# Optimization experiments

Hardware: AMD Instinct MI355X
Metric: run time of the kernel (lower is better)

Reference implementation:

```python
import jax, jax.numpy as jnp
import numpy as np

DT = 10.0          # ms per step
T_STEPS = 120      # rollout length
THRESHOLD = 0.5
MIX = 0.0          # competition_mix (buffer, default 0.0)
EPS_TOTAL = 1e-6
EPS_SLOPE = 1e-3
NOISE_SEED = 42


def setup_inputs() -> dict:
    key = jax.random.key(0)
    B, C = 65536, 4
    logits = jax.random.normal(key, (B, C), dtype=jnp.float32)
    return {
        "logits": logits,
        "input_scale": jnp.float32(0.25),
        "leak": jnp.full((C,), 0.08, dtype=jnp.float32),
        "self_excitation": jnp.full((C,), 0.12, dtype=jnp.float32),
        "inhibition": jnp.float32(0.08),
        "competition_gain": jnp.float32(1.0),
        "noise_std": jnp.float32(0.02),
        "evidence_w": jnp.float32(1.0),   # evidence_proj: Linear(1,1) weight
        "evidence_b": jnp.float32(0.0),   # evidence_proj bias
    }


def _forward(logits, input_scale, leak, self_excitation, inhibition,
             competition_gain, noise_std, evidence_w, evidence_b):
    B, C = logits.shape
    # momentary evidence: scale, center, softplus, 1x1 linear
    centered = logits * input_scale
    centered = centered - jnp.mean(centered, axis=1, keepdims=True)
    evidence = jax.nn.softplus(centered) * evidence_w + evidence_b  # (B, C)

    lk = jax.nn.softplus(leak)                # (C,)
    se = jax.nn.softplus(self_excitation)     # (C,)
    inhib = jax.nn.softplus(inhibition)       # ()
    cgain = jax.nn.softplus(competition_gain) # ()
    nstd = jax.nn.softplus(noise_std)         # ()

    keys = jax.random.split(jax.random.key(NOISE_SEED), T_STEPS)

    def step(acc, k):
        total = jnp.sum(acc, axis=1, keepdims=True)      # (B, 1)
        total_other = total - acc                        # (B, C)
        normalized_other = total_other / (total + EPS_TOTAL)
        competition = (1.0 - MIX) * total_other + MIX * cgain * normalized_other
        drive = evidence + se * acc - inhib * competition - lk * acc
        noise = jax.random.normal(k, (B, C), dtype=jnp.float32) * nstd
        dsdt = jax.nn.softplus(drive + noise) - acc
        acc_new = jnp.maximum(acc + 0.2 * dsdt, 0.0)     # clamp(min=0)
        return acc_new, (acc_new, dsdt)

    acc0 = jnp.zeros((B, C), dtype=jnp.float32)
    _, (traj, dsdt_traj) = jax.lax.scan(step, acc0, keys)
    traj = jnp.transpose(traj, (1, 0, 2))           # (B, T, C)
    dsdt_traj = jnp.transpose(dsdt_traj, (1, 0, 2)) # (B, T, C)

    # DiffDecisionMultiClass: first threshold crossing per class, with
    # linear interpolation using dsdt (slope = 0.2*dsdt per step) so the
    # decision time is differentiable via the implicit-function gradient.
    diff = traj - THRESHOLD                          # (B, T, C)
    crossed = diff > 0.0
    any_c = jnp.any(crossed, axis=1)                 # (B, C)
    idx = jnp.argmax(crossed, axis=1)                # (B, C) first crossing step
    idx = jnp.where(any_c, idx, T_STEPS - 1)

    diff_c = jnp.take_along_axis(diff, idx[:, None, :], axis=1)[:, 0, :]       # (B, C)
    slope = 0.2 * jnp.take_along_axis(dsdt_traj, idx[:, None, :], axis=1)[:, 0, :]
    slope_safe = jnp.where(slope >= 0.0,
                           jnp.maximum(slope, EPS_SLOPE),
                           jnp.minimum(slope, -EPS_SLOPE))
    # continuous crossing time in steps (gradient flows through diff_c only)
    t_cont = idx.astype(jnp.float32) - diff_c / jax.lax.stop_gradient(slope_safe)
    times_ms = jnp.where(any_c, t_cont * DT, jnp.float32(T_STEPS * DT))
    return times_ms / 1000.0  # seconds, (B, C)


def reference(logits, input_scale, leak, self_excitation, inhibition,
              competition_gain, noise_std, evidence_w, evidence_b):
    return _forward(logits, input_scale, leak, self_excitation, inhibition,
                    competition_gain, noise_std, evidence_w, evidence_b)
```

## Files before the change

kernel.cpp:

```cpp
#include <hip/hip_runtime.h>
#include <cstdint>

#define TSTEPS 120

__device__ __forceinline__ uint32_t rotl32(uint32_t x, uint32_t r) {
    return (x << r) | (x >> (32u - r));
}

__device__ __forceinline__ void tf2x32_pair(uint32_t ks0, uint32_t ks1, uint32_t ks2,
                                            uint32_t xa1, uint32_t xb1,
                                            uint32_t &oa, uint32_t &ob) {
    uint32_t a0 = ks0, a1 = xa1 + ks1;
    uint32_t b0 = ks0, b1 = xb1 + ks1;
#define R2(r) { a0 += a1; a1 = rotl32(a1, r); a1 ^= a0; \
                b0 += b1; b1 = rotl32(b1, r); b1 ^= b0; }
    R2(13u) R2(15u) R2(26u) R2(6u)
    a0 += ks1; a1 += ks2 + 1u;  b0 += ks1; b1 += ks2 + 1u;
    R2(17u) R2(29u) R2(16u) R2(24u)
    a0 += ks2; a1 += ks0 + 2u;  b0 += ks2; b1 += ks0 + 2u;
    R2(13u) R2(15u) R2(26u) R2(6u)
    a0 += ks0; a1 += ks1 + 3u;  b0 += ks0; b1 += ks1 + 3u;
    R2(17u) R2(29u) R2(16u) R2(24u)
    a0 += ks1; a1 += ks2 + 4u;  b0 += ks1; b1 += ks2 + 4u;
    R2(13u) R2(15u) R2(26u) R2(6u)
    a0 += ks2; a1 += ks0 + 5u;  b0 += ks2; b1 += ks0 + 5u;
#undef R2
    oa = a0 ^ a1; ob = b0 ^ b1;
}

__device__ __forceinline__ float softplus_fast(float x) {
    const float LOG2E = 1.4426950408889634f;
    const float LN2   = 0.6931471805599453f;
    float e = __builtin_amdgcn_exp2f(-fabsf(x) * LOG2E);
    float l = __builtin_amdgcn_logf(1.0f + e) * LN2;
    return fmaxf(x, 0.0f) + l;
}

__device__ __forceinline__ float erfinv_fast(float x) {
    const float LN2 = 0.6931471805599453f;
    float t = 1.0f - x * x;
    float w = -(__builtin_amdgcn_logf(t) * LN2);
    float wa = w - 2.5f;
    float wb = __builtin_amdgcn_sqrtf(w) - 3.0f;
    float pa = 2.81022636e-08f, pb = -0.000200214257f;
    pa = fmaf(pa, wa, 3.43273939e-07f);  pb = fmaf(pb, wb, 0.000100950558f);
    pa = fmaf(pa, wa, -3.5233877e-06f);  pb = fmaf(pb, wb, 0.00134934322f);
    pa = fmaf(pa, wa, -4.39150654e-06f); pb = fmaf(pb, wb, -0.00367342844f);
    pa = fmaf(pa, wa, 0.00021858087f);   pb = fmaf(pb, wb, 0.00573950773f);
    pa = fmaf(pa, wa, -0.00125372503f);  pb = fmaf(pb, wb, -0.0076224613f);
    pa = fmaf(pa, wa, -0.00417768164f);  pb = fmaf(pb, wb, 0.00943887047f);
    pa = fmaf(pa, wa, 0.246640727f);     pb = fmaf(pb, wb, 1.00167406f);
    pa = fmaf(pa, wa, 1.50140941f);      pb = fmaf(pb, wb, 2.83297682f);
    float p = (w < 5.0f) ? pa : pb;
    return p * x;
}

__global__ __launch_bounds__(256) void accrace_kernel(
    const float* __restrict__ logits,
    const float* __restrict__ g_input_scale,
    const float* __restrict__ g_leak,
    const float* __restrict__ g_se,
    const float* __restrict__ g_inhib,
    const float* __restrict__ g_nstd,
    const float* __restrict__ g_ew,
    const float* __restrict__ g_eb,
    float* __restrict__ out, int n)
{
    __shared__ uint32_t kw0[TSTEPS], kw1[TSTEPS];
    const int tid = threadIdx.x;
    if (tid < TSTEPS) {
        uint32_t o0, o1;
        const uint32_t k0 = 0u, k1 = 42u;
        uint32_t x0 = 0u, x1 = (uint32_t)tid;
        uint32_t ks2 = k0 ^ k1 ^ 0x1BD11BDAu;
        x0 += k0; x1 += k1;
#define TF_R(r) { x0 += x1; x1 = rotl32(x1, r); x1 ^= x0; }
        TF_R(13u) TF_R(15u) TF_R(26u) TF_R(6u)
        x0 += k1; x1 += ks2 + 1u;
        TF_R(17u) TF_R(29u) TF_R(16u) TF_R(24u)
        x0 += ks2; x1 += k0 + 2u;
        TF_R(13u) TF_R(15u) TF_R(26u) TF_R(6u)
        x0 += k0; x1 += k1 + 3u;
        TF_R(17u) TF_R(29u) TF_R(16u) TF_R(24u)
        x0 += k1; x1 += ks2 + 4u;
        TF_R(13u) TF_R(15u) TF_R(26u) TF_R(6u)
        x0 += ks2; x1 += k0 + 5u;
#undef TF_R
        kw0[tid] = x0; kw1[tid] = x1;
    }
    __syncthreads();

    const int base = blockIdx.x * 512;
    const int jA = base + tid;
    const int jB = base + 256 + tid;
    if (jB >= n) return;
    const int c = tid & 3;

    const float input_scale = g_input_scale[0];
    const float lkc   = softplus_fast(g_leak[c]);
    const float sec   = softplus_fast(g_se[c]);
    const float inhib = softplus_fast(g_inhib[0]);
    const float nstd  = softplus_fast(g_nstd[0]);
    const float ew = g_ew[0], eb = g_eb[0];

    const float xsA = logits[jA] * input_scale;
    const float xsB = logits[jB] * input_scale;
    const float sA1 = xsA + __shfl_xor(xsA, 1, 64);
    const float sB1 = xsB + __shfl_xor(xsB, 1, 64);
    const float sA  = sA1 + __shfl_xor(sA1, 2, 64);
    const float sB  = sB1 + __shfl_xor(sB1, 2, 64);
    const float evdA = softplus_fast(xsA - sA * 0.25f) * ew + eb;
    const float evdB = softplus_fast(xsB - sB * 0.25f) * ew + eb;

    const float LO    = -0.99999994f;
    const float RANGE = 2.0f;
    const float SQRT2 = 1.41421356237309515f;

    float accA = 0.0f, diffA = 0.0f, slopeA = 0.0f;
    float accB = 0.0f, diffB = 0.0f, slopeB = 0.0f;
    int idxA = -1, idxB = -1;
    const uint32_t ctrA = (uint32_t)jA, ctrB = (uint32_t)jB;

    uint32_t nbA, nbB;
    {
        const uint32_t k0 = kw0[0], k1 = kw1[0];
        tf2x32_pair(k0, k1, k0 ^ k1 ^ 0x1BD11BDAu, ctrA, ctrB, nbA, nbB);
    }

    for (int t = 0; t < TSTEPS; ++t) {
        const uint32_t bitsA = nbA, bitsB = nbB;
        if (t + 1 < TSTEPS) {
            const uint32_t k0 = kw0[t + 1], k1 = kw1[t + 1];
            tf2x32_pair(k0, k1, k0 ^ k1 ^ 0x1BD11BDAu, ctrA, ctrB, nbA, nbB);
        }

        const float tA1 = accA + __shfl_xor(accA, 1, 64);
        const float tB1 = accB + __shfl_xor(accB, 1, 64);
        const float totA = tA1 + __shfl_xor(tA1, 2, 64);
        const float totB = tB1 + __shfl_xor(tB1, 2, 64);

        const float fA = __uint_as_float((bitsA >> 9) | 0x3F800000u) - 1.0f;
        const float fB = __uint_as_float((bitsB >> 9) | 0x3F800000u) - 1.0f;
        const float uA = fmaxf(LO, fA * RANGE + LO);
        const float uB = fmaxf(LO, fB * RANGE + LO);
        const float nzA = (SQRT2 * erfinv_fast(uA)) * nstd;
        const float nzB = (SQRT2 * erfinv_fast(uB)) * nstd;

        const float toA = totA - accA;
        const float toB = totB - accB;
        const float drA = evdA + sec * accA - inhib * toA - lkc * accA;
        const float drB = evdB + sec * accB - inhib * toB - lkc * accB;
        const float dsA = softplus_fast(drA + nzA) - accA;
        const float dsB = softplus_fast(drB + nzB) - accB;
        const float anA = fmaxf(accA + 0.2f * dsA, 0.0f);
        const float anB = fmaxf(accB + 0.2f * dsB, 0.0f);

        const bool crA = (idxA < 0) && (anA > 0.5f);
        const bool crB = (idxB < 0) && (anB > 0.5f);
        idxA   = crA ? t : idxA;            idxB   = crB ? t : idxB;
        diffA  = crA ? anA - 0.5f : diffA;  diffB  = crB ? anB - 0.5f : diffB;
        slopeA = crA ? 0.2f * dsA : slopeA; slopeB = crB ? 0.2f * dsB : slopeB;
        accA = anA; accB = anB;
    }

    float oA, oB;
    if (idxA >= 0) {
        const float ss = (slopeA >= 0.0f) ? fmaxf(slopeA, 1e-3f) : fminf(slopeA, -1e-3f);
        oA = (((float)idxA - diffA / ss) * 10.0f) / 1000.0f;
    } else oA = 1.2f;
    if (idxB >= 0) {
        const float ss = (slopeB >= 0.0f) ? fmaxf(slopeB, 1e-3f) : fminf(slopeB, -1e-3f);
        oB = (((float)idxB - diffB / ss) * 10.0f) / 1000.0f;
    } else oB = 1.2f;
    out[jA] = oA;
    out[jB] = oB;
}

extern "C" void kernel_launch(void* const* d_in, const int* in_sizes, int n_in,
                              void* d_out, int out_size, void* d_ws, size_t ws_size,
                              hipStream_t stream) {
    const float* logits       = (const float*)d_in[0];
    const float* input_scale  = (const float*)d_in[1];
    const float* leak         = (const float*)d_in[2];
    const float* self_excit   = (const float*)d_in[3];
    const float* inhibition   = (const float*)d_in[4];
    const float* noise_std    = (const float*)d_in[6];
    const float* evidence_w   = (const float*)d_in[7];
    const float* evidence_b   = (const float*)d_in[8];

    const int n = in_sizes[0];
    const int threads = 256;
    const int blocks = (n + 2 * threads - 1) / (2 * threads);
    accrace_kernel<<<blocks, threads, 0, stream>>>(
        logits, input_scale, leak, self_excit, inhibition,
        noise_std, evidence_w, evidence_b, (float*)d_out, n);
}
```

Baseline: 102.7 us.

## Vectorize the accumulator step with packed float2 math and DPP quad reductions

The per-step math for the two rows each thread owns now uses two-wide float vectors so the compiler can emit packed FMA instructions. The lane-xor shuffles become DPP quad permutes, the Threefry keys are made wave-uniform with readfirstlane and prefetched two steps ahead, and the drive expression is folded into fewer FMAs. The erfinv tail polynomial is evaluated only when some lane in the wave needs it, and the loop is unrolled by two. These aim to cut VALU and cross-lane instruction count, at the cost of a divergent branch and slight changes in rounding from the algebraic refolding.

```diff
diff --git a/kernel.cpp b/kernel.cpp
--- a/kernel.cpp
+++ b/kernel.cpp
@@ -3,56 +3,93 @@
 
 #define TSTEPS 120
 
-__device__ __forceinline__ uint32_t rotl32(uint32_t x, uint32_t r) {
-    return (x << r) | (x >> (32u - r));
-}
-
-__device__ __forceinline__ void tf2x32_pair(uint32_t ks0, uint32_t ks1, uint32_t ks2,
-                                            uint32_t xa1, uint32_t xb1,
-                                            uint32_t &oa, uint32_t &ob) {
-    uint32_t a0 = ks0, a1 = xa1 + ks1;
-    uint32_t b0 = ks0, b1 = xb1 + ks1;
-#define R2(r) { a0 += a1; a1 = rotl32(a1, r); a1 ^= a0; \
-                b0 += b1; b1 = rotl32(b1, r); b1 ^= b0; }
+typedef float f32x2 __attribute__((ext_vector_type(2)));
+typedef unsigned int u32;
+
+__device__ __forceinline__ u32 rotl32(u32 x, u32 r) { return (x << r) | (x >> (32u - r)); }
+
+__device__ __forceinline__ f32x2 splat2(float v) { f32x2 r; r.x = v; r.y = v; return r; }
+__device__ __forceinline__ f32x2 fma2(f32x2 a, f32x2 b, f32x2 c) {
+    return __builtin_elementwise_fma(a, b, c);
+}
+
+__device__ __forceinline__ float qxor1(float x) {
+    return __int_as_float(__builtin_amdgcn_update_dpp(0, __float_as_int(x), 0xB1, 0xF, 0xF, true));
+}
+__device__ __forceinline__ float qxor2(float x) {
+    return __int_as_float(__builtin_amdgcn_update_dpp(0, __float_as_int(x), 0x4E, 0xF, 0xF, true));
+}
+
+__device__ __forceinline__ float softplus_s(float x) {
+    const float LOG2E = 1.4426950408889634f, LN2 = 0.6931471805599453f;
+    float e = __builtin_amdgcn_exp2f(-fabsf(x) * LOG2E);
+    return fmaxf(x, 0.0f) + __builtin_amdgcn_logf(1.0f + e) * LN2;
+}
+
+__device__ __forceinline__ f32x2 softplus2(f32x2 x) {
+    const float LOG2E = 1.4426950408889634f, LN2 = 0.6931471805599453f;
+    f32x2 t = __builtin_elementwise_abs(x) * splat2(-LOG2E);
+    f32x2 e; e.x = __builtin_amdgcn_exp2f(t.x); e.y = __builtin_amdgcn_exp2f(t.y);
+    f32x2 e1 = e + splat2(1.0f);
+    f32x2 l; l.x = __builtin_amdgcn_logf(e1.x); l.y = __builtin_amdgcn_logf(e1.y);
+    f32x2 mx = __builtin_elementwise_max(x, splat2(0.0f));
+    return fma2(l, splat2(LN2), mx);
+}
+
+__device__ __forceinline__ f32x2 erfinv2(f32x2 x) {
+    const float LN2 = 0.6931471805599453f;
+    f32x2 t = fma2(-x, x, splat2(1.0f));
+    f32x2 w;
+    w.x = __builtin_amdgcn_logf(t.x) * (-LN2);
+    w.y = __builtin_amdgcn_logf(t.y) * (-LN2);
+    f32x2 wa = w - splat2(2.5f);
+    f32x2 p = splat2(2.81022636e-08f);
+    p = fma2(p, wa, splat2(3.43273939e-07f));
+    p = fma2(p, wa, splat2(-3.5233877e-06f));
+    p = fma2(p, wa, splat2(-4.39150654e-06f));
+    p = fma2(p, wa, splat2(0.00021858087f));
+    p = fma2(p, wa, splat2(-0.00125372503f));
+    p = fma2(p, wa, splat2(-0.00417768164f));
+    p = fma2(p, wa, splat2(0.246640727f));
+    p = fma2(p, wa, splat2(1.50140941f));
+    if (__any((w.x >= 5.0f) || (w.y >= 5.0f))) {
+        f32x2 wb;
+        wb.x = __builtin_amdgcn_sqrtf(w.x) - 3.0f;
+        wb.y = __builtin_amdgcn_sqrtf(w.y) - 3.0f;
+        f32x2 q = splat2(-0.000200214257f);
+        q = fma2(q, wb, splat2(0.000100950558f));
+        q = fma2(q, wb, splat2(0.00134934322f));
+        q = fma2(q, wb, splat2(-0.00367342844f));
+        q = fma2(q, wb, splat2(0.00573950773f));
+        q = fma2(q, wb, splat2(-0.0076224613f));
+        q = fma2(q, wb, splat2(0.00943887047f));
+        q = fma2(q, wb, splat2(1.00167406f));
+        q = fma2(q, wb, splat2(2.83297682f));
+        p.x = (w.x < 5.0f) ? p.x : q.x;
+        p.y = (w.y < 5.0f) ? p.y : q.y;
+    }
+    return p * x;
+}
+
+__device__ __forceinline__ void tf_pair(u32 k0, u32 k1, u32 cA, u32 cB, u32 &oa, u32 &ob) {
+    const u32 ks2 = k0 ^ k1 ^ 0x1BD11BDAu;
+    const u32 i1 = ks2 + 1u, i2 = k0 + 2u, i3 = k1 + 3u, i4 = ks2 + 4u, i5 = k0 + 5u;
+    u32 a0 = k0, a1 = cA + k1;
+    u32 b0 = k0, b1 = cB + k1;
+#define R2(r) { a0 += a1; a1 = rotl32(a1,(r)); a1 ^= a0; \
+                b0 += b1; b1 = rotl32(b1,(r)); b1 ^= b0; }
     R2(13u) R2(15u) R2(26u) R2(6u)
-    a0 += ks1; a1 += ks2 + 1u;  b0 += ks1; b1 += ks2 + 1u;
+    a0 += k1;  a1 += i1;  b0 += k1;  b1 += i1;
     R2(17u) R2(29u) R2(16u) R2(24u)
-    a0 += ks2; a1 += ks0 + 2u;  b0 += ks2; b1 += ks0 + 2u;
+    a0 += ks2; a1 += i2;  b0 += ks2; b1 += i2;
     R2(13u) R2(15u) R2(26u) R2(6u)
-    a0 += ks0; a1 += ks1 + 3u;  b0 += ks0; b1 += ks1 + 3u;
+    a0 += k0;  a1 += i3;  b0 += k0;  b1 += i3;
     R2(17u) R2(29u) R2(16u) R2(24u)
-    a0 += ks1; a1 += ks2 + 4u;  b0 += ks1; b1 += ks2 + 4u;
+    a0 += k1;  a1 += i4;  b0 += k1;  b1 += i4;
     R2(13u) R2(15u) R2(26u) R2(6u)
-    a0 += ks2; a1 += ks0 + 5u;  b0 += ks2; b1 += ks0 + 5u;
+    a0 += ks2; a1 += i5;  b0 += ks2; b1 += i5;
 #undef R2
     oa = a0 ^ a1; ob = b0 ^ b1;
-}
-
-__device__ __forceinline__ float softplus_fast(float x) {
-    const float LOG2E = 1.4426950408889634f;
-    const float LN2   = 0.6931471805599453f;
-    float e = __builtin_amdgcn_exp2f(-fabsf(x) * LOG2E);
-    float l = __builtin_amdgcn_logf(1.0f + e) * LN2;
-    return fmaxf(x, 0.0f) + l;
-}
-
-__device__ __forceinline__ float erfinv_fast(float x) {
-    const float LN2 = 0.6931471805599453f;
-    float t = 1.0f - x * x;
-    float w = -(__builtin_amdgcn_logf(t) * LN2);
-    float wa = w - 2.5f;
-    float wb = __builtin_amdgcn_sqrtf(w) - 3.0f;
-    float pa = 2.81022636e-08f, pb = -0.000200214257f;
-    pa = fmaf(pa, wa, 3.43273939e-07f);  pb = fmaf(pb, wb, 0.000100950558f);
-    pa = fmaf(pa, wa, -3.5233877e-06f);  pb = fmaf(pb, wb, 0.00134934322f);
-    pa = fmaf(pa, wa, -4.39150654e-06f); pb = fmaf(pb, wb, -0.00367342844f);
-    pa = fmaf(pa, wa, 0.00021858087f);   pb = fmaf(pb, wb, 0.00573950773f);
-    pa = fmaf(pa, wa, -0.00125372503f);  pb = fmaf(pb, wb, -0.0076224613f);
-    pa = fmaf(pa, wa, -0.00417768164f);  pb = fmaf(pb, wb, 0.00943887047f);
-    pa = fmaf(pa, wa, 0.246640727f);     pb = fmaf(pb, wb, 1.00167406f);
-    pa = fmaf(pa, wa, 1.50140941f);      pb = fmaf(pb, wb, 2.83297682f);
-    float p = (w < 5.0f) ? pa : pb;
-    return p * x;
 }
 
 __global__ __launch_bounds__(256) void accrace_kernel(
@@ -66,23 +103,21 @@
     const float* __restrict__ g_eb,
     float* __restrict__ out, int n)
 {
-    __shared__ uint32_t kw0[TSTEPS], kw1[TSTEPS];
+    __shared__ u32 kw0[TSTEPS], kw1[TSTEPS];
     const int tid = threadIdx.x;
     if (tid < TSTEPS) {
-        uint32_t o0, o1;
-        const uint32_t k0 = 0u, k1 = 42u;
-        uint32_t x0 = 0u, x1 = (uint32_t)tid;
-        uint32_t ks2 = k0 ^ k1 ^ 0x1BD11BDAu;
-        x0 += k0; x1 += k1;
-#define TF_R(r) { x0 += x1; x1 = rotl32(x1, r); x1 ^= x0; }
+        const u32 k0 = 0u, k1 = 42u;
+        const u32 ks2 = k0 ^ k1 ^ 0x1BD11BDAu;
+        u32 x0 = k0, x1 = (u32)tid + k1;
+#define TF_R(r) { x0 += x1; x1 = rotl32(x1,(r)); x1 ^= x0; }
         TF_R(13u) TF_R(15u) TF_R(26u) TF_R(6u)
-        x0 += k1; x1 += ks2 + 1u;
+        x0 += k1;  x1 += ks2 + 1u;
         TF_R(17u) TF_R(29u) TF_R(16u) TF_R(24u)
         x0 += ks2; x1 += k0 + 2u;
         TF_R(13u) TF_R(15u) TF_R(26u) TF_R(6u)
-        x0 += k0; x1 += k1 + 3u;
+        x0 += k0;  x1 += k1 + 3u;
         TF_R(17u) TF_R(29u) TF_R(16u) TF_R(24u)
-        x0 += k1; x1 += ks2 + 4u;
+        x0 += k1;  x1 += ks2 + 4u;
         TF_R(13u) TF_R(15u) TF_R(26u) TF_R(6u)
         x0 += ks2; x1 += k0 + 5u;
 #undef TF_R
@@ -97,80 +132,83 @@
     const int c = tid & 3;
 
     const float input_scale = g_input_scale[0];
-    const float lkc   = softplus_fast(g_leak[c]);
-    const float sec   = softplus_fast(g_se[c]);
-    const float inhib = softplus_fast(g_inhib[0]);
-    const float nstd  = softplus_fast(g_nstd[0]);
+    const float lkc   = softplus_s(g_leak[c]);
+    const float sec   = softplus_s(g_se[c]);
+    const float inhib = softplus_s(g_inhib[0]);
+    const float nstd  = softplus_s(g_nstd[0]);
     const float ew = g_ew[0], eb = g_eb[0];
+
+    const float gain   = sec + inhib - lkc;
+    const float minhib = -inhib;
+    const float SQ2N   = 1.41421356237309515f * nstd;
+    const float LO     = -0.99999994f;
 
     const float xsA = logits[jA] * input_scale;
     const float xsB = logits[jB] * input_scale;
-    const float sA1 = xsA + __shfl_xor(xsA, 1, 64);
-    const float sB1 = xsB + __shfl_xor(xsB, 1, 64);
-    const float sA  = sA1 + __shfl_xor(sA1, 2, 64);
-    const float sB  = sB1 + __shfl_xor(sB1, 2, 64);
-    const float evdA = softplus_fast(xsA - sA * 0.25f) * ew + eb;
-    const float evdB = softplus_fast(xsB - sB * 0.25f) * ew + eb;
-
-    const float LO    = -0.99999994f;
-    const float RANGE = 2.0f;
-    const float SQRT2 = 1.41421356237309515f;
-
-    float accA = 0.0f, diffA = 0.0f, slopeA = 0.0f;
-    float accB = 0.0f, diffB = 0.0f, slopeB = 0.0f;
-    int idxA = -1, idxB = -1;
-    const uint32_t ctrA = (uint32_t)jA, ctrB = (uint32_t)jB;
-
-    uint32_t nbA, nbB;
+    float mA = xsA + qxor1(xsA); mA = (mA + qxor2(mA)) * 0.25f;
+    float mB = xsB + qxor1(xsB); mB = (mB + qxor2(mB)) * 0.25f;
+    f32x2 evd; evd.x = softplus_s(xsA - mA) * ew + eb;
+               evd.y = softplus_s(xsB - mB) * ew + eb;
+
+    const u32 ctrA = (u32)jA, ctrB = (u32)jB;
+
+    u32 nbA, nbB;
     {
-        const uint32_t k0 = kw0[0], k1 = kw1[0];
-        tf2x32_pair(k0, k1, k0 ^ k1 ^ 0x1BD11BDAu, ctrA, ctrB, nbA, nbB);
-    }
-
+        u32 k0 = (u32)__builtin_amdgcn_readfirstlane((int)kw0[0]);
+        u32 k1 = (u32)__builtin_amdgcn_readfirstlane((int)kw1[0]);
+        tf_pair(k0, k1, ctrA, ctrB, nbA, nbB);
+    }
+    u32 pk0 = kw0[1], pk1 = kw1[1];
+
+    f32x2 acc = splat2(0.0f);
+    f32x2 tfx = splat2(-1.0f);
+    f32x2 dfx = splat2(0.0f);
+    f32x2 slx = splat2(0.0f);
+    float tcur = 0.0f;
+
+#pragma unroll 2
     for (int t = 0; t < TSTEPS; ++t) {
-        const uint32_t bitsA = nbA, bitsB = nbB;
-        if (t + 1 < TSTEPS) {
-            const uint32_t k0 = kw0[t + 1], k1 = kw1[t + 1];
-            tf2x32_pair(k0, k1, k0 ^ k1 ^ 0x1BD11BDAu, ctrA, ctrB, nbA, nbB);
+        const u32 bitsA = nbA, bitsB = nbB;
+        {
+            u32 k0 = (u32)__builtin_amdgcn_readfirstlane((int)pk0);
+            u32 k1 = (u32)__builtin_amdgcn_readfirstlane((int)pk1);
+            tf_pair(k0, k1, ctrA, ctrB, nbA, nbB);
         }
-
-        const float tA1 = accA + __shfl_xor(accA, 1, 64);
-        const float tB1 = accB + __shfl_xor(accB, 1, 64);
-        const float totA = tA1 + __shfl_xor(tA1, 2, 64);
-        const float totB = tB1 + __shfl_xor(tB1, 2, 64);
-
-        const float fA = __uint_as_float((bitsA >> 9) | 0x3F800000u) - 1.0f;
-        const float fB = __uint_as_float((bitsB >> 9) | 0x3F800000u) - 1.0f;
-        const float uA = fmaxf(LO, fA * RANGE + LO);
-        const float uB = fmaxf(LO, fB * RANGE + LO);
-        const float nzA = (SQRT2 * erfinv_fast(uA)) * nstd;
-        const float nzB = (SQRT2 * erfinv_fast(uB)) * nstd;
-
-        const float toA = totA - accA;
-        const float toB = totB - accB;
-        const float drA = evdA + sec * accA - inhib * toA - lkc * accA;
-        const float drB = evdB + sec * accB - inhib * toB - lkc * accB;
-        const float dsA = softplus_fast(drA + nzA) - accA;
-        const float dsB = softplus_fast(drB + nzB) - accB;
-        const float anA = fmaxf(accA + 0.2f * dsA, 0.0f);
-        const float anB = fmaxf(accB + 0.2f * dsB, 0.0f);
-
-        const bool crA = (idxA < 0) && (anA > 0.5f);
-        const bool crB = (idxB < 0) && (anB > 0.5f);
-        idxA   = crA ? t : idxA;            idxB   = crB ? t : idxB;
-        diffA  = crA ? anA - 0.5f : diffA;  diffB  = crB ? anB - 0.5f : diffB;
-        slopeA = crA ? 0.2f * dsA : slopeA; slopeB = crB ? 0.2f * dsB : slopeB;
-        accA = anA; accB = anB;
+        const int tn2 = (t + 2 < TSTEPS) ? t + 2 : TSTEPS - 1;
+        pk0 = kw0[tn2]; pk1 = kw1[tn2];
+
+        f32x2 s1, tot;
+        s1.x = acc.x + qxor1(acc.x);  s1.y = acc.y + qxor1(acc.y);
+        tot.x = s1.x + qxor2(s1.x);   tot.y = s1.y + qxor2(s1.y);
+
+        f32x2 fr;
+        fr.x = __uint_as_float((bitsA >> 9) | 0x3F800000u);
+        fr.y = __uint_as_float((bitsB >> 9) | 0x3F800000u);
+        f32x2 f = fr - splat2(1.0f);
+        f32x2 u = __builtin_elementwise_max(fma2(f, splat2(2.0f), splat2(LO)), splat2(LO));
+        f32x2 nz = erfinv2(u) * splat2(SQ2N);
+
+        f32x2 dr = fma2(acc, splat2(gain), fma2(tot, splat2(minhib), evd));
+        f32x2 ds = softplus2(dr + nz) - acc;
+        f32x2 an = __builtin_elementwise_max(fma2(ds, splat2(0.2f), acc), splat2(0.0f));
+
+        const bool cA = (tfx.x < 0.0f) && (an.x > 0.5f);
+        const bool cB = (tfx.y < 0.0f) && (an.y > 0.5f);
+        tfx.x = cA ? tcur : tfx.x;  dfx.x = cA ? an.x : dfx.x;  slx.x = cA ? ds.x : slx.x;
+        tfx.y = cB ? tcur : tfx.y;  dfx.y = cB ? an.y : dfx.y;  slx.y = cB ? ds.y : slx.y;
+        acc = an; tcur += 1.0f;
     }
 
     float oA, oB;
-    if (idxA >= 0) {
-        const float ss = (slopeA >= 0.0f) ? fmaxf(slopeA, 1e-3f) : fminf(slopeA, -1e-3f);
-        oA = (((float)idxA - diffA / ss) * 10.0f) / 1000.0f;
+    if (tfx.x >= 0.0f) {
+        const float sl = 0.2f * slx.x;
+        const float ss = (sl >= 0.0f) ? fmaxf(sl, 1e-3f) : fminf(sl, -1e-3f);
+        oA = ((tfx.x - (dfx.x - 0.5f) / ss) * 10.0f) / 1000.0f;
     } else oA = 1.2f;
-    if (idxB >= 0) {
-        const float ss = (slopeB >= 0.0f) ? fmaxf(slopeB, 1e-3f) : fminf(slopeB, -1e-3f);
-        oB = (((float)idxB - diffB / ss) * 10.0f) / 1000.0f;
+    if (tfx.y >= 0.0f) {
+        const float sl = 0.2f * slx.y;
+        const float ss = (sl >= 0.0f) ? fmaxf(sl, 1e-3f) : fminf(sl, -1e-3f);
+        oB = ((tfx.y - (dfx.y - 0.5f) / ss) * 10.0f) / 1000.0f;
     } else oB = 1.2f;
     out[jA] = oA;
     out[jB] = oB;
```

Result: faster. 93.63 us (-8.8%).
